# Kernel optimization log

Measured on AMD Instinct MI355X. Metric: run time of the kernel, lower is better.

## Reference

```python
import jax, jax.numpy as jnp
import numpy as np

B, S, H, H2, NH, K, L, V, TOUT, MEL = 16, 256, 384, 1536, 2, 3, 4, 256, 1024, 80


def _ln(x, sb):
    # sb: [2, H] -> (scale, bias)
    m = x.mean(-1, keepdims=True)
    v = x.var(-1, keepdims=True)
    return (x - m) * jax.lax.rsqrt(v + 1e-5) * sb[0] + sb[1]


def _conv1d(x, w, b):
    # x: [B, T, Cin], w: [K, Cin, Cout]
    return jax.lax.conv_general_dilated(x, w, (1,), 'SAME',
                                         dimension_numbers=('NWC', 'WIO', 'NWC')) + b


def _mha(x, w, b):
    # w: [4, H, H] (q, k, v, o), b: [4, H]
    T = x.shape[1]
    dh = H // NH
    q = (x @ w[0] + b[0]).reshape(B, T, NH, dh)
    k = (x @ w[1] + b[1]).reshape(B, T, NH, dh)
    v = (x @ w[2] + b[2]).reshape(B, T, NH, dh)
    s = jnp.einsum('bqhd,bkhd->bhqk', q, k) / np.sqrt(dh).astype(np.float32)
    a = jax.nn.softmax(s, axis=-1)
    o = jnp.einsum('bhqk,bkhd->bqhd', a, v).reshape(B, T, H)
    return o @ w[3] + b[3]


def _fft_block(x, aw, ab, c1w, c1b, c2w, c2b, ln):
    x = _ln(x + _mha(x, aw, ab), ln[0])
    f = _conv1d(jax.nn.relu(_conv1d(x, c1w, c1b)), c2w, c2b)
    return _ln(x + f, ln[1])


def _posenc(x):
    T = x.shape[1]
    pos = jnp.arange(T, dtype=jnp.float32)[:, None]
    den = jnp.exp(-np.log(10000.0) * jnp.arange(0, H, 2, dtype=jnp.float32) / H)
    ang = pos * den[None, :]
    pe = jnp.stack([jnp.sin(ang), jnp.cos(ang)], axis=-1).reshape(T, H)
    return x + pe[None]


def setup_inputs() -> dict:
    key = jax.random.key(0)
    ks = iter(jax.random.split(key, 32))
    sc = 0.02
    inp = {}
    inp['tokens'] = jax.random.randint(next(ks), (B, S), 0, V, dtype=jnp.int32)
    inp['alignes'] = jax.random.randint(next(ks), (B, S), 0, 8).astype(jnp.int64)
    inp['tok_emb'] = jax.random.normal(next(ks), (V, H), jnp.float32) * sc
    for pre in ('enc', 'dec'):
        inp[pre + '_attn_w'] = jax.random.normal(next(ks), (L, 4, H, H), jnp.float32) * sc
        inp[pre + '_attn_b'] = jnp.zeros((L, 4, H), jnp.float32)
        inp[pre + '_conv1_w'] = jax.random.normal(next(ks), (L, K, H, H2), jnp.float32) * sc
        inp[pre + '_conv1_b'] = jnp.zeros((L, H2), jnp.float32)
        inp[pre + '_conv2_w'] = jax.random.normal(next(ks), (L, K, H2, H), jnp.float32) * sc
        inp[pre + '_conv2_b'] = jnp.zeros((L, H), jnp.float32)
        ln = jnp.stack([jnp.ones((L, 2, H)), jnp.zeros((L, 2, H))], axis=2)  # [L,2,2,H]
        inp[pre + '_ln'] = ln.astype(jnp.float32)
    inp['al_conv1_w'] = jax.random.normal(next(ks), (K, H, H), jnp.float32) * sc
    inp['al_conv1_b'] = jnp.zeros((H,), jnp.float32)
    inp['al_conv2_w'] = jax.random.normal(next(ks), (K, H, H), jnp.float32) * sc
    inp['al_conv2_b'] = jnp.zeros((H,), jnp.float32)
    inp['al_ln'] = jnp.stack([jnp.ones((2, H)), jnp.zeros((2, H))], axis=1).astype(jnp.float32)
    inp['al_lin_w'] = jax.random.normal(next(ks), (H, 1), jnp.float32) * sc
    inp['al_lin_b'] = jnp.zeros((1,), jnp.float32)
    inp['dec_lin_w'] = jax.random.normal(next(ks), (H, MEL), jnp.float32) * sc
    inp['dec_lin_b'] = jnp.zeros((MEL,), jnp.float32)
    return inp


def reference(tokens, alignes, tok_emb, enc_attn_w, enc_attn_b, enc_conv1_w,
              enc_conv1_b, enc_conv2_w, enc_conv2_b, enc_ln, dec_attn_w,
              dec_attn_b, dec_conv1_w, dec_conv1_b, dec_conv2_w, dec_conv2_b,
              dec_ln, al_conv1_w, al_conv1_b, al_conv2_w, al_conv2_b, al_ln,
              al_lin_w, al_lin_b, dec_lin_w, dec_lin_b):
    # ---- Encoder ----
    x = tok_emb[tokens] * np.sqrt(H).astype(np.float32)
    x = _posenc(x)
    for i in range(L):
        x = _fft_block(x, enc_attn_w[i], enc_attn_b[i], enc_conv1_w[i],
                       enc_conv1_b[i], enc_conv2_w[i], enc_conv2_b[i], enc_ln[i])
    # ---- Aligner (duration predictor) ----
    h = jax.nn.relu(_conv1d(x, al_conv1_w, al_conv1_b))
    h = _ln(h, al_ln[0])
    h = jax.nn.relu(_conv1d(h, al_conv2_w, al_conv2_b))
    h = _ln(h, al_ln[1])
    length_pred = (h @ al_lin_w + al_lin_b)[..., 0]  # [B, S]
    # ---- Length regulator: repeat_interleave + pad_sequence (static TOUT) ----
    dur = alignes.astype(jnp.int32)
    cum = jnp.cumsum(dur, axis=1)                    # [B, S]
    t = jnp.arange(TOUT, dtype=jnp.int32)
    idx = jax.vmap(lambda c: jnp.searchsorted(c, t, side='right'))(cum)  # [B, TOUT]
    valid = t[None, :] < cum[:, -1:]
    idx = jnp.clip(idx, 0, S - 1)
    expanded = jnp.take_along_axis(x, idx[:, :, None], axis=1)
    expanded = expanded * valid[:, :, None].astype(x.dtype)
    # ---- Decoder ----
    y = _posenc(expanded)
    for i in range(L):
        y = _fft_block(y, dec_attn_w[i], dec_attn_b[i], dec_conv1_w[i],
                       dec_conv1_b[i], dec_conv2_w[i], dec_conv2_b[i], dec_ln[i])
    mel = y @ dec_lin_w + dec_lin_b                  # [B, TOUT, 80]
    return jnp.transpose(mel, (0, 2, 1)), length_pred
```

## Files before the change

### kernel.cpp

```cpp
#include <hip/hip_runtime.h>
#include <cstdint>
#include <cstddef>

#define B_    16
#define S_    256
#define H_    384
#define H2_   1536
#define NH_   2
#define DH_   192
#define TOUT_ 1024
#define MEL_  80
#define L_    4

#define F_BIAS  1
#define F_RES   2
#define F_RELU  4
#define F_STF   8
#define F_STB   16
#define F_TRANS 32

typedef __attribute__((ext_vector_type(8))) short short8;
typedef __attribute__((ext_vector_type(4))) float floatx4;

typedef const __attribute__((address_space(1))) unsigned int* as1p;
typedef __attribute__((address_space(3))) unsigned int* as3p;

__device__ __forceinline__ void gld16(const void* g, void* l) {
  __builtin_amdgcn_global_load_lds((as1p)g, (as3p)l, 16, 0, 0);
}

__device__ __forceinline__ short f2b(float f) {
  union { float f; unsigned u; } v; v.f = f;
  unsigned r = (v.u + 0x7fffu + ((v.u >> 16) & 1u)) >> 16;
  return (short)r;
}

__device__ __forceinline__ float pe_val(int t, int i) {
  int j = i >> 1;
  float den = __expf(-9.210340371976184f * (float)(2 * j) / (float)H_);
  float ang = (float)t * den;
  return (i & 1) ? __cosf(ang) : __sinf(ang);
}

__global__ __launch_bounds__(256) void wtrans_kernel(const float* __restrict__ sa,
                                                     const float* __restrict__ sb,
                                                     int na, int K, int N,
                                                     short* __restrict__ dst) {
  __shared__ float t[32][33];
  int id = blockIdx.z;
  const float* s = (id < na) ? sa + (size_t)id * K * N : sb + (size_t)(id - na) * K * N;
  short* o = dst + (size_t)id * K * N;
  int n0 = blockIdx.x * 32, k0 = blockIdx.y * 32;
  int tx = threadIdx.x & 31, ty = threadIdx.x >> 5;
#pragma unroll
  for (int i = 0; i < 4; ++i)
    t[ty + i * 8][tx] = s[(size_t)(k0 + ty + i * 8) * N + n0 + tx];
  __syncthreads();
#pragma unroll
  for (int i = 0; i < 4; ++i)
    o[(size_t)(n0 + ty + i * 8) * K + k0 + tx] = f2b(t[tx][ty + i * 8]);
}

__global__ void melpad_kernel(const float* __restrict__ w, short* __restrict__ dst) {
  int i = blockIdx.x * 256 + threadIdx.x;
  int n = i / H_, k = i - n * H_;
  dst[i] = (n < MEL_) ? f2b(w[(size_t)k * MEL_ + n]) : (short)0;
}

__global__ void embed_kernel(const int* __restrict__ tokens, const float* __restrict__ emb,
                             float* __restrict__ xf, short* __restrict__ xb) {
  int bs = blockIdx.x;
  int t  = bs & (S_ - 1);
  int tok = tokens[bs];
  const float* e = emb + (size_t)tok * H_;
  float* of = xf + (size_t)bs * H_;
  short* ob = xb + (size_t)bs * H_;
  for (int i = threadIdx.x; i < H_; i += blockDim.x) {
    float v = e[i] * 19.595917942265423f + pe_val(t, i);
    of[i] = v; ob[i] = f2b(v);
  }
}

template<int NTAPS>
__global__ __launch_bounds__(256) void mfma_gemm(
    const short* __restrict__ A, const short* __restrict__ Wt,
    const float* __restrict__ bias, const float* __restrict__ res,
    float* __restrict__ Cf, short* __restrict__ Cb, const short* __restrict__ zbuf,
    int M, int N, int Kd, int T, int Nout, int flags)
{
  constexpr int HB   = NTAPS / 2;
  constexpr int RA   = 128 + NTAPS - 1;
  constexpr int RNDA = (RA + 63) / 64;
  __shared__ __align__(16) short As[RA * 32];
  __shared__ __align__(16) short Bs[NTAPS * 128 * 32];
  const int tid = threadIdx.x;
  const int wave = tid >> 6, lane = tid & 63, quad = lane >> 4, lm = lane & 15;
  const int bm = blockIdx.y * 128, bn = blockIdx.x * 128;
  const int wm = (wave >> 1) * 64, wn = (wave & 1) * 64;
  const int b0 = bm / T, t0 = bm - b0 * T;
  floatx4 acc[4][4] = {};

  for (int k0 = 0; k0 < Kd; k0 += 32) {
#pragma unroll
    for (int j = 0; j < RNDA; ++j) {
      int r0 = (j == RNDA - 1) ? (RA - 64) : j * 64;
      int r = r0 + (tid >> 2);
      int t = t0 - HB + r;
      const short* g = (t >= 0 && t < T)
          ? (A + (size_t)(b0 * T + t) * Kd + k0 + (tid & 3) * 8) : zbuf;
      gld16(g, As + r0 * 32 + wave * 512);
    }
#pragma unroll
    for (int j = 0; j < 2 * NTAPS; ++j) {
      int gi = j * 256 + tid;
      int tap = gi >> 9, rr = (gi >> 2) & 127, ch = gi & 3;
      const short* g = Wt + ((size_t)tap * N + bn + rr) * Kd + k0 + ch * 8;
      gld16(g, Bs + j * 2048 + wave * 512);
    }
    __syncthreads();
#pragma unroll
    for (int tap = 0; tap < NTAPS; ++tap) {
      short8 af[4], bfr[4];
#pragma unroll
      for (int mt = 0; mt < 4; ++mt)
        af[mt] = *(const short8*)(&As[(wm + mt * 16 + lm + tap) * 32 + quad * 8]);
#pragma unroll
      for (int nt = 0; nt < 4; ++nt)
        bfr[nt] = *(const short8*)(&Bs[tap * 4096 + (wn + nt * 16 + lm) * 32 + quad * 8]);
#pragma unroll
      for (int mt = 0; mt < 4; ++mt)
#pragma unroll
        for (int nt = 0; nt < 4; ++nt)
          acc[mt][nt] = __builtin_amdgcn_mfma_f32_16x16x32_bf16(af[mt], bfr[nt],
                                                                acc[mt][nt], 0, 0, 0);
    }
    __syncthreads();
  }

#pragma unroll
  for (int mt = 0; mt < 4; ++mt) {
#pragma unroll
    for (int r2 = 0; r2 < 4; ++r2) {
      int gm = bm + wm + mt * 16 + quad * 4 + r2;
#pragma unroll
      for (int nt = 0; nt < 4; ++nt) {
        int gn = bn + wn + nt * 16 + lm;
        float v = acc[mt][nt][r2];
        if (flags & F_TRANS) {
          if (gn < Nout) {
            if (flags & F_BIAS) v += bias[gn];
            int bb = gm / T, tt = gm - bb * T;
            Cf[((size_t)bb * Nout + gn) * T + tt] = v;
          }
          continue;
        }
        if (flags & F_BIAS) v += bias[gn];
        size_t idx = (size_t)gm * N + gn;
        if (flags & F_RES) v += res[idx];
        if (flags & F_RELU) v = fmaxf(v, 0.f);
        if (flags & F_STF) Cf[idx] = v;
        if (flags & F_STB) Cb[idx] = f2b(v);
      }
    }
  }
}

__global__ __launch_bounds__(256) void vtrans_kernel(const short* __restrict__ qkv,
                                                     short* __restrict__ vt, int T) {
  __shared__ short tile[32][34];
  int b = blockIdx.z, d0 = blockIdx.y * 32, t0 = blockIdx.x * 32;
  int tx = threadIdx.x & 31, ty = threadIdx.x >> 5;
#pragma unroll
  for (int i = 0; i < 4; ++i)
    tile[ty + i * 8][tx] = qkv[(size_t)(b * T + t0 + ty + i * 8) * 1152 + 768 + d0 + tx];
  __syncthreads();
  int h = (d0 >= DH_) ? 1 : 0;
  int dd0 = d0 - h * DH_;
#pragma unroll
  for (int i = 0; i < 4; ++i)
    vt[((size_t)((b * NH_ + h) * DH_) + dd0 + ty + i * 8) * T + t0 + tx] = tile[tx][ty + i * 8];
}

template<int T>
__global__ __launch_bounds__(256) void attn_mfma(const short* __restrict__ qkv,
                                                 const short* __restrict__ vt,
                                                 short* __restrict__ o)
{
  constexpr int PK = T / 64;
  constexpr int PW = T + 8;
  __shared__ __align__(16) short qs[16 * 200];
  __shared__ __align__(16) short P[16 * PW];
  __shared__ float red[4][16];
  const int tid = threadIdx.x;
  const int wave = tid >> 6, lane = tid & 63, quad = lane >> 4, lm = lane & 15;
  const int q0 = blockIdx.x * 16, h = blockIdx.y, b = blockIdx.z;
  const short* qb = qkv + (size_t)b * T * 1152 + h * DH_;
  const short* kb = qb + 384;
  const short* vb = vt + (size_t)(b * NH_ + h) * DH_ * T;

  for (int u = tid; u < 16 * 24; u += 256) {
    int r = u / 24, c = u - r * 24;
    *(int4*)(qs + r * 200 + c * 8) = *(const int4*)(qb + (size_t)(q0 + r) * 1152 + c * 8);
  }
  __syncthreads();

  short8 qf[6];
#pragma unroll
  for (int c6 = 0; c6 < 6; ++c6)
    qf[c6] = *(const short8*)(qs + lm * 200 + c6 * 32 + quad * 8);

  floatx4 sacc[PK];
#pragma unroll
  for (int i = 0; i < PK; ++i) {
    int kt = i * 4 + wave;
    floatx4 a = {0.f, 0.f, 0.f, 0.f};
    const short* kp = kb + (size_t)(kt * 16 + lm) * 1152 + quad * 8;
#pragma unroll
    for (int c6 = 0; c6 < 6; ++c6)
      a = __builtin_amdgcn_mfma_f32_16x16x32_bf16(qf[c6], *(const short8*)(kp + c6 * 32),
                                                  a, 0, 0, 0);
#pragma unroll
    for (int r2 = 0; r2 < 4; ++r2) a[r2] *= 0.07216878364870323f;
    sacc[i] = a;
  }

  float mx[4];
#pragma unroll
  for (int r2 = 0; r2 < 4; ++r2) {
    float m = sacc[0][r2];
#pragma unroll
    for (int i = 1; i < PK; ++i) m = fmaxf(m, sacc[i][r2]);
#pragma unroll
    for (int off = 1; off < 16; off <<= 1) m = fmaxf(m, __shfl_xor(m, off, 64));
    mx[r2] = m;
  }
  if (lm == 0) {
#pragma unroll
    for (int r2 = 0; r2 < 4; ++r2) red[wave][quad * 4 + r2] = mx[r2];
  }
  __syncthreads();
  float gm[4];
#pragma unroll
  for (int r2 = 0; r2 < 4; ++r2) {
    int row = quad * 4 + r2;
    gm[r2] = fmaxf(fmaxf(red[0][row], red[1][row]), fmaxf(red[2][row], red[3][row]));
  }
  __syncthreads();

  float sm[4] = {0.f, 0.f, 0.f, 0.f};
#pragma unroll
  for (int i = 0; i < PK; ++i) {
#pragma unroll
    for (int r2 = 0; r2 < 4; ++r2) {
      float e = __expf(sacc[i][r2] - gm[r2]);
      sm[r2] += e;
      P[(quad * 4 + r2) * PW + (i * 4 + wave) * 16 + lm] = f2b(e);
    }
  }
#pragma unroll
  for (int r2 = 0; r2 < 4; ++r2) {
#pragma unroll
    for (int off = 1; off < 16; off <<= 1) sm[r2] += __shfl_xor(sm[r2], off, 64);
  }
  if (lm == 0) {
#pragma unroll
    for (int r2 = 0; r2 < 4; ++r2) red[wave][quad * 4 + r2] = sm[r2];
  }
  __syncthreads();
  float il[4];
#pragma unroll
  for (int r2 = 0; r2 < 4; ++r2) {
    int row = quad * 4 + r2;
    il[r2] = 1.f / (red[0][row] + red[1][row] + red[2][row] + red[3][row]);
  }

  floatx4 oacc[3] = {};
  for (int kc = 0; kc < T / 32; ++kc) {
    short8 af = *(const short8*)(P + lm * PW + kc * 32 + quad * 8);
#pragma unroll
    for (int dx = 0; dx < 3; ++dx) {
      short8 bf = *(const short8*)(vb + (size_t)((wave + dx * 4) * 16 + lm) * T + kc * 32 + quad * 8);
      oacc[dx] = __builtin_amdgcn_mfma_f32_16x16x32_bf16(af, bf, oacc[dx], 0, 0, 0);
    }
  }
#pragma unroll
  for (int dx = 0; dx < 3; ++dx) {
    int col = h * DH_ + (wave + dx * 4) * 16 + lm;
#pragma unroll
    for (int r2 = 0; r2 < 4; ++r2)
      o[(size_t)(b * T + q0 + quad * 4 + r2) * H_ + col] = f2b(oacc[dx][r2] * il[r2]);
  }
}

__global__ __launch_bounds__(256) void ln_kernel(const float* __restrict__ X,
                                                 const float* __restrict__ sb,
                                                 float* __restrict__ Yf,
                                                 short* __restrict__ Yb, int M)
{
  int row  = blockIdx.x * 4 + (threadIdx.x >> 6);
  int lane = threadIdx.x & 63;
  const float* x = X + (size_t)row * H_;
  float v[6]; float s = 0.f, ss = 0.f;
#pragma unroll
  for (int i = 0; i < 6; ++i) { v[i] = x[lane + i * 64]; s += v[i]; ss += v[i] * v[i]; }
#pragma unroll
  for (int o = 32; o; o >>= 1) { s += __shfl_down(s, o, 64); ss += __shfl_down(ss, o, 64); }
  s = __shfl(s, 0, 64); ss = __shfl(ss, 0, 64);
  float mean = s * (1.0f / H_);
  float var  = ss * (1.0f / H_) - mean * mean;
  float r = rsqrtf(var + 1e-5f);
  float* yf = Yf + (size_t)row * H_;
#pragma unroll
  for (int i = 0; i < 6; ++i) {
    int c = lane + i * 64;
    float y = (v[i] - mean) * r * sb[c] + sb[H_ + c];
    yf[c] = y;
    if (Yb) Yb[(size_t)row * H_ + c] = f2b(y);
  }
}

__global__ void gemv_kernel(const float* __restrict__ A, const float* __restrict__ w,
                            const float* __restrict__ bflt, float* __restrict__ out, int M)
{
  int row  = blockIdx.x * 4 + (threadIdx.x >> 6);
  int lane = threadIdx.x & 63;
  const float* a = A + (size_t)row * H_;
  float s = 0.f;
#pragma unroll
  for (int i = 0; i < 6; ++i) s += a[lane + i * 64] * w[lane + i * 64];
#pragma unroll
  for (int o = 32; o; o >>= 1) s += __shfl_down(s, o, 64);
  if (lane == 0) out[row] = s + bflt[0];
}

__global__ void cumsum_kernel(const int* __restrict__ al, int* __restrict__ cum) {
  int b = threadIdx.x;
  if (b < B_) {
    int acc = 0;
    for (int s = 0; s < S_; ++s) { acc += al[b * S_ + s]; cum[b * S_ + s] = acc; }
  }
}

__global__ void expand_kernel(const float* __restrict__ xe, const int* __restrict__ cum,
                              float* __restrict__ yf, short* __restrict__ yb) {
  int t = blockIdx.x, b = blockIdx.y;
  const int* c = cum + b * S_;
  int lo = 0, hi = S_;
  while (lo < hi) { int mid = (lo + hi) >> 1; if (c[mid] <= t) lo = mid + 1; else hi = mid; }
  int idx = lo < S_ ? lo : S_ - 1;
  bool valid = t < c[S_ - 1];
  const float* src = xe + ((size_t)b * S_ + idx) * H_;
  float* df = yf + ((size_t)b * TOUT_ + t) * H_;
  short* db = yb + ((size_t)b * TOUT_ + t) * H_;
  for (int i = threadIdx.x; i < H_; i += blockDim.x) {
    float v = (valid ? src[i] : 0.f) + pe_val(t, i);
    df[i] = v; db[i] = f2b(v);
  }
}

static inline void gemm(const short* A, const short* Wt, const float* bias, const float* res,
                        float* Cf, short* Cb, const short* zbuf, int M, int N, int Kd, int T,
                        int ntaps, int Nout, int flags, hipStream_t st) {
  dim3 g(N / 128, M / 128);
  if (ntaps == 3)
    mfma_gemm<3><<<g, 256, 0, st>>>(A, Wt, bias, res, Cf, Cb, zbuf, M, N, Kd, T, Nout, flags);
  else
    mfma_gemm<1><<<g, 256, 0, st>>>(A, Wt, bias, res, Cf, Cb, zbuf, M, N, Kd, T, Nout, flags);
}

struct LayerW { const short *attn, *c1, *c2; const float *ab, *c1b, *c2b, *ln; };

static void fft_block(float* x, short* xb, short* qkvb, short* ob, short* vtb, short* h2b,
                      const short* zbuf, const LayerW& w, int T, hipStream_t st)
{
  int M = B_ * T;
  const size_t msz = (size_t)H_ * H_;
  gemm(xb, w.attn, w.ab, nullptr, nullptr, qkvb, zbuf, M, 1152, H_, T, 1, 0, F_BIAS | F_STB, st);
  vtrans_kernel<<<dim3(T / 32, 12, B_), 256, 0, st>>>(qkvb, vtb, T);
  if (T == 256) attn_mfma<256><<<dim3(T / 16, NH_, B_), 256, 0, st>>>(qkvb, vtb, ob);
  else          attn_mfma<1024><<<dim3(T / 16, NH_, B_), 256, 0, st>>>(qkvb, vtb, ob);
  gemm(ob, w.attn + 3 * msz, w.ab + 3 * H_, x, x, nullptr, zbuf, M, H_, H_, T, 1, 0,
       F_BIAS | F_RES | F_STF, st);
  ln_kernel<<<M / 4, 256, 0, st>>>(x, w.ln, x, xb, M);
  gemm(xb, w.c1, w.c1b, nullptr, nullptr, h2b, zbuf, M, H2_, H_, T, 3, 0,
       F_BIAS | F_RELU | F_STB, st);
  gemm(h2b, w.c2, w.c2b, x, x, nullptr, zbuf, M, H_, H2_, T, 3, 0, F_BIAS | F_RES | F_STF, st);
  ln_kernel<<<M / 4, 256, 0, st>>>(x, w.ln + 2 * H_, x, xb, M);
}

extern "C" void kernel_launch(void* const* d_in, const int* in_sizes, int n_in,
                              void* d_out, int out_size, void* d_ws, size_t ws_size,
                              hipStream_t stream)
{
  (void)in_sizes; (void)n_in; (void)out_size; (void)ws_size;
  const int*   tokens      = (const int*)d_in[0];
  const int*   alignes     = (const int*)d_in[1];
  const float* tok_emb     = (const float*)d_in[2];
  const float* enc_attn_w  = (const float*)d_in[3];
  const float* enc_attn_b  = (const float*)d_in[4];
  const float* enc_conv1_w = (const float*)d_in[5];
  const float* enc_conv1_b = (const float*)d_in[6];
  const float* enc_conv2_w = (const float*)d_in[7];
  const float* enc_conv2_b = (const float*)d_in[8];
  const float* enc_ln      = (const float*)d_in[9];
  const float* dec_attn_w  = (const float*)d_in[10];
  const float* dec_attn_b  = (const float*)d_in[11];
  const float* dec_conv1_w = (const float*)d_in[12];
  const float* dec_conv1_b = (const float*)d_in[13];
  const float* dec_conv2_w = (const float*)d_in[14];
  const float* dec_conv2_b = (const float*)d_in[15];
  const float* dec_ln      = (const float*)d_in[16];
  const float* al_c1w      = (const float*)d_in[17];
  const float* al_c1b      = (const float*)d_in[18];
  const float* al_c2w      = (const float*)d_in[19];
  const float* al_c2b      = (const float*)d_in[20];
  const float* al_ln       = (const float*)d_in[21];
  const float* al_lin_w    = (const float*)d_in[22];
  const float* al_lin_b    = (const float*)d_in[23];
  const float* dec_lin_w   = (const float*)d_in[24];
  const float* dec_lin_b   = (const float*)d_in[25];

  char* base = (char*)d_ws;
  size_t off = 0;
  auto alloc = [&](size_t bytes) -> char* {
    char* p = base + off;
    off += (bytes + 255) & ~(size_t)255;
    return p;
  };
  const size_t ME = (size_t)B_ * S_;
  const size_t MD = (size_t)B_ * TOUT_;
  float* xe   = (float*)alloc(ME * H_ * 4);
  short* xeb  = (short*)alloc(ME * H_ * 2);
  float* xd   = (float*)alloc(MD * H_ * 4);
  short* xdb  = (short*)alloc(MD * H_ * 2);
  short* qkvb = (short*)alloc(MD * 1152 * 2);
  short* ob   = (short*)alloc(MD * H_ * 2);
  short* h2b  = (short*)alloc(MD * H2_ * 2);
  short* vtb  = h2b;
  short* wAt  = (short*)alloc((size_t)32 * H_ * H_ * 2);
  short* wAl  = (short*)alloc((size_t)6 * H_ * H_ * 2);
  short* wC1  = (short*)alloc((size_t)24 * H_ * H2_ * 2);
  short* wC2  = (short*)alloc((size_t)24 * H_ * H2_ * 2);
  short* wMel = (short*)alloc((size_t)128 * H_ * 2);
  int*   cum  = (int*)alloc(ME * 4);
  short* zbuf = (short*)alloc(256);
  float* alf  = xd;
  short* alb  = xdb;

  float* mel_out = (float*)d_out;
  float* len_out = mel_out + (size_t)B_ * MEL_ * TOUT_;

  hipMemsetAsync(zbuf, 0, 256, stream);

  wtrans_kernel<<<dim3(12, 12, 32), 256, 0, stream>>>(enc_attn_w, dec_attn_w, 16, H_, H_, wAt);
  wtrans_kernel<<<dim3(12, 12, 6),  256, 0, stream>>>(al_c1w, al_c2w, 3, H_, H_, wAl);
  wtrans_kernel<<<dim3(48, 12, 24), 256, 0, stream>>>(enc_conv1_w, dec_conv1_w, 12, H_, H2_, wC1);
  wtrans_kernel<<<dim3(12, 48, 24), 256, 0, stream>>>(enc_conv2_w, dec_conv2_w, 12, H2_, H_, wC2);
  melpad_kernel<<<dim3(128 * H_ / 256), 256, 0, stream>>>(dec_lin_w, wMel);

  embed_kernel<<<dim3(B_ * S_), 128, 0, stream>>>(tokens, tok_emb, xe, xeb);
  for (int i = 0; i < L_; ++i) {
    LayerW w;
    w.attn = wAt + (size_t)i * 4 * H_ * H_;
    w.c1   = wC1 + (size_t)i * 3 * H_ * H2_;
    w.c2   = wC2 + (size_t)i * 3 * H_ * H2_;
    w.ab   = enc_attn_b + (size_t)i * 4 * H_;
    w.c1b  = enc_conv1_b + (size_t)i * H2_;
    w.c2b  = enc_conv2_b + (size_t)i * H_;
    w.ln   = enc_ln + (size_t)i * 4 * H_;
    fft_block(xe, xeb, qkvb, ob, vtb, h2b, zbuf, w, S_, stream);
  }

  {
    int Ma = B_ * S_;
    gemm(xeb, wAl, al_c1b, nullptr, alf, nullptr, zbuf, Ma, H_, H_, S_, 3, 0,
         F_BIAS | F_RELU | F_STF, stream);
    ln_kernel<<<Ma / 4, 256, 0, stream>>>(alf, al_ln, alf, alb, Ma);
    gemm(alb, wAl + (size_t)3 * H_ * H_, al_c2b, nullptr, alf, nullptr, zbuf, Ma, H_, H_, S_,
         3, 0, F_BIAS | F_RELU | F_STF, stream);
    ln_kernel<<<Ma / 4, 256, 0, stream>>>(alf, al_ln + 2 * H_, alf, (short*)nullptr, Ma);
    gemv_kernel<<<Ma / 4, 256, 0, stream>>>(alf, al_lin_w, al_lin_b, len_out, Ma);
  }

  cumsum_kernel<<<1, 64, 0, stream>>>(alignes, cum);
  expand_kernel<<<dim3(TOUT_, B_), 128, 0, stream>>>(xe, cum, xd, xdb);

  for (int i = 0; i < L_; ++i) {
    LayerW w;
    w.attn = wAt + (size_t)(16 + i * 4) * H_ * H_;
    w.c1   = wC1 + (size_t)(12 + i * 3) * H_ * H2_;
    w.c2   = wC2 + (size_t)(12 + i * 3) * H_ * H2_;
    w.ab   = dec_attn_b + (size_t)i * 4 * H_;
    w.c1b  = dec_conv1_b + (size_t)i * H2_;
    w.c2b  = dec_conv2_b + (size_t)i * H_;
    w.ln   = dec_ln + (size_t)i * 4 * H_;
    fft_block(xd, xdb, qkvb, ob, vtb, h2b, zbuf, w, TOUT_, stream);
  }

  gemm(xdb, wMel, dec_lin_b, nullptr, mel_out, nullptr, zbuf, B_ * TOUT_, 128, H_, TOUT_,
       1, MEL_, F_BIAS | F_TRANS, stream);
}
```

Before: 3.363 ms.

## Replace attention kernel with flash-style online softmax and double-buffered K/V staging

The attention kernel now gives each block 64 queries, with 16 per wave, and streams K and V in 32-key chunks. Each chunk is double-buffered in LDS through async global loads, and the softmax is computed online with a running max and sum per row. The old kernel handled 16 queries per block, read K and V straight from global memory, and held the full score row in LDS. The new layout gives four times more K/V reuse per block, removes the full-row LDS buffer, and overlaps loads with MFMA work. In exchange, each wave holds 12 output accumulators, which raises register pressure, and the block count drops, which may lower occupancy and parallelism for the short encoder sequence.

```diff
diff --git a/kernel.cpp b/kernel.cpp
--- a/kernel.cpp
+++ b/kernel.cpp
@@ -182,113 +182,111 @@
 }
 
 template<int T>
-__global__ __launch_bounds__(256) void attn_mfma(const short* __restrict__ qkv,
-                                                 const short* __restrict__ vt,
-                                                 short* __restrict__ o)
+__global__ __launch_bounds__(256) void attn_flash(const short* __restrict__ qkv,
+                                                  const short* __restrict__ vt,
+                                                  short* __restrict__ o)
 {
-  constexpr int PK = T / 64;
-  constexpr int PW = T + 8;
-  __shared__ __align__(16) short qs[16 * 200];
-  __shared__ __align__(16) short P[16 * PW];
-  __shared__ float red[4][16];
+  constexpr int NKT = T / 32;
+  __shared__ __align__(16) short Kb[2][6144];
+  __shared__ __align__(16) short Vb[2][6144];
+  __shared__ __align__(16) short Pb[4][16 * 40];
   const int tid = threadIdx.x;
   const int wave = tid >> 6, lane = tid & 63, quad = lane >> 4, lm = lane & 15;
-  const int q0 = blockIdx.x * 16, h = blockIdx.y, b = blockIdx.z;
+  const int id = blockIdx.x;
+  const int bh = id & 31, h = bh & 1, b = bh >> 1;
+  const int q0 = (id >> 5) * 64;
   const short* qb = qkv + (size_t)b * T * 1152 + h * DH_;
   const short* kb = qb + 384;
   const short* vb = vt + (size_t)(b * NH_ + h) * DH_ * T;
 
-  for (int u = tid; u < 16 * 24; u += 256) {
-    int r = u / 24, c = u - r * 24;
-    *(int4*)(qs + r * 200 + c * 8) = *(const int4*)(qb + (size_t)(q0 + r) * 1152 + c * 8);
-  }
+  short8 qf[6];
+  {
+    const short* qrow = qb + (size_t)(q0 + wave * 16 + lm) * 1152 + quad * 8;
+#pragma unroll
+    for (int c6 = 0; c6 < 6; ++c6) qf[c6] = *(const short8*)(qrow + c6 * 32);
+  }
+
+  auto stage = [&](int kc, int bi) {
+#pragma unroll
+    for (int j = 0; j < 3; ++j) {
+      int g = j * 256 + tid;
+      int lmg = g & 15, qg = (g >> 4) & 3, ct = g >> 6;
+      int c6 = ct % 6, kt = ct / 6;
+      gld16(kb + (size_t)(kc * 32 + kt * 16 + lmg) * 1152 + c6 * 32 + qg * 8,
+            &Kb[bi][j * 2048 + wave * 512]);
+    }
+#pragma unroll
+    for (int j = 0; j < 3; ++j) {
+      int g = j * 256 + tid;
+      int lmg = g & 15, qg = (g >> 4) & 3, dt = g >> 6;
+      gld16(vb + (size_t)(dt * 16 + lmg) * T + kc * 32 + qg * 8,
+            &Vb[bi][j * 2048 + wave * 512]);
+    }
+  };
+
+  float m_r[4] = {-1e30f, -1e30f, -1e30f, -1e30f};
+  float l_r[4] = {0.f, 0.f, 0.f, 0.f};
+  floatx4 oacc[12] = {};
+
+  stage(0, 0);
   __syncthreads();
 
-  short8 qf[6];
-#pragma unroll
-  for (int c6 = 0; c6 < 6; ++c6)
-    qf[c6] = *(const short8*)(qs + lm * 200 + c6 * 32 + quad * 8);
-
-  floatx4 sacc[PK];
-#pragma unroll
-  for (int i = 0; i < PK; ++i) {
-    int kt = i * 4 + wave;
-    floatx4 a = {0.f, 0.f, 0.f, 0.f};
-    const short* kp = kb + (size_t)(kt * 16 + lm) * 1152 + quad * 8;
-#pragma unroll
-    for (int c6 = 0; c6 < 6; ++c6)
-      a = __builtin_amdgcn_mfma_f32_16x16x32_bf16(qf[c6], *(const short8*)(kp + c6 * 32),
-                                                  a, 0, 0, 0);
-#pragma unroll
-    for (int r2 = 0; r2 < 4; ++r2) a[r2] *= 0.07216878364870323f;
-    sacc[i] = a;
-  }
-
-  float mx[4];
+  for (int kc = 0; kc < NKT; ++kc) {
+    const int cur = kc & 1;
+    if (kc + 1 < NKT) stage(kc + 1, cur ^ 1);
+
+    floatx4 s0 = {0.f, 0.f, 0.f, 0.f}, s1 = {0.f, 0.f, 0.f, 0.f};
+#pragma unroll
+    for (int c6 = 0; c6 < 6; ++c6) {
+      short8 k0f = *(const short8*)(&Kb[cur][(c6 * 64 + quad * 16 + lm) * 8]);
+      short8 k1f = *(const short8*)(&Kb[cur][((6 + c6) * 64 + quad * 16 + lm) * 8]);
+      s0 = __builtin_amdgcn_mfma_f32_16x16x32_bf16(qf[c6], k0f, s0, 0, 0, 0);
+      s1 = __builtin_amdgcn_mfma_f32_16x16x32_bf16(qf[c6], k1f, s1, 0, 0, 0);
+    }
+
+    float al[4];
+#pragma unroll
+    for (int r2 = 0; r2 < 4; ++r2) {
+      float a = s0[r2] * 0.07216878364870323f;
+      float c = s1[r2] * 0.07216878364870323f;
+      float t = fmaxf(a, c);
+#pragma unroll
+      for (int off = 1; off < 16; off <<= 1) t = fmaxf(t, __shfl_xor(t, off, 64));
+      float mn = fmaxf(m_r[r2], t);
+      al[r2] = __expf(m_r[r2] - mn);
+      m_r[r2] = mn;
+      float e0 = __expf(a - mn), e1 = __expf(c - mn);
+      l_r[r2] = al[r2] * l_r[r2] + e0 + e1;
+      Pb[wave][(quad * 4 + r2) * 40 + lm]      = f2b(e0);
+      Pb[wave][(quad * 4 + r2) * 40 + 16 + lm] = f2b(e1);
+    }
+#pragma unroll
+    for (int dt = 0; dt < 12; ++dt) {
+#pragma unroll
+      for (int r2 = 0; r2 < 4; ++r2) oacc[dt][r2] *= al[r2];
+    }
+
+    short8 pf = *(const short8*)(&Pb[wave][lm * 40 + quad * 8]);
+#pragma unroll
+    for (int dt = 0; dt < 12; ++dt) {
+      short8 vf = *(const short8*)(&Vb[cur][(dt * 64 + quad * 16 + lm) * 8]);
+      oacc[dt] = __builtin_amdgcn_mfma_f32_16x16x32_bf16(pf, vf, oacc[dt], 0, 0, 0);
+    }
+    __syncthreads();
+  }
+
 #pragma unroll
   for (int r2 = 0; r2 < 4; ++r2) {
-    float m = sacc[0][r2];
-#pragma unroll
-    for (int i = 1; i < PK; ++i) m = fmaxf(m, sacc[i][r2]);
-#pragma unroll
-    for (int off = 1; off < 16; off <<= 1) m = fmaxf(m, __shfl_xor(m, off, 64));
-    mx[r2] = m;
-  }
-  if (lm == 0) {
-#pragma unroll
-    for (int r2 = 0; r2 < 4; ++r2) red[wave][quad * 4 + r2] = mx[r2];
-  }
-  __syncthreads();
-  float gm[4];
-#pragma unroll
-  for (int r2 = 0; r2 < 4; ++r2) {
-    int row = quad * 4 + r2;
-    gm[r2] = fmaxf(fmaxf(red[0][row], red[1][row]), fmaxf(red[2][row], red[3][row]));
-  }
-  __syncthreads();
-
-  float sm[4] = {0.f, 0.f, 0.f, 0.f};
-#pragma unroll
-  for (int i = 0; i < PK; ++i) {
-#pragma unroll
-    for (int r2 = 0; r2 < 4; ++r2) {
-      float e = __expf(sacc[i][r2] - gm[r2]);
-      sm[r2] += e;
-      P[(quad * 4 + r2) * PW + (i * 4 + wave) * 16 + lm] = f2b(e);
-    }
-  }
-#pragma unroll
-  for (int r2 = 0; r2 < 4; ++r2) {
-#pragma unroll
-    for (int off = 1; off < 16; off <<= 1) sm[r2] += __shfl_xor(sm[r2], off, 64);
-  }
-  if (lm == 0) {
-#pragma unroll
-    for (int r2 = 0; r2 < 4; ++r2) red[wave][quad * 4 + r2] = sm[r2];
-  }
-  __syncthreads();
-  float il[4];
-#pragma unroll
-  for (int r2 = 0; r2 < 4; ++r2) {
-    int row = quad * 4 + r2;
-    il[r2] = 1.f / (red[0][row] + red[1][row] + red[2][row] + red[3][row]);
-  }
-
-  floatx4 oacc[3] = {};
-  for (int kc = 0; kc < T / 32; ++kc) {
-    short8 af = *(const short8*)(P + lm * PW + kc * 32 + quad * 8);
-#pragma unroll
-    for (int dx = 0; dx < 3; ++dx) {
-      short8 bf = *(const short8*)(vb + (size_t)((wave + dx * 4) * 16 + lm) * T + kc * 32 + quad * 8);
-      oacc[dx] = __builtin_amdgcn_mfma_f32_16x16x32_bf16(af, bf, oacc[dx], 0, 0, 0);
-    }
-  }
-#pragma unroll
-  for (int dx = 0; dx < 3; ++dx) {
-    int col = h * DH_ + (wave + dx * 4) * 16 + lm;
+#pragma unroll
+    for (int off = 1; off < 16; off <<= 1) l_r[r2] += __shfl_xor(l_r[r2], off, 64);
+    l_r[r2] = 1.f / l_r[r2];
+  }
+  short* orow = o + (size_t)(b * T + q0 + wave * 16) * H_ + h * DH_;
+#pragma unroll
+  for (int dt = 0; dt < 12; ++dt) {
 #pragma unroll
     for (int r2 = 0; r2 < 4; ++r2)
-      o[(size_t)(b * T + q0 + quad * 4 + r2) * H_ + col] = f2b(oacc[dx][r2] * il[r2]);
+      orow[(size_t)(quad * 4 + r2) * H_ + dt * 16 + lm] = f2b(oacc[dt][r2] * l_r[r2]);
   }
 }
 
@@ -377,8 +375,8 @@
   const size_t msz = (size_t)H_ * H_;
   gemm(xb, w.attn, w.ab, nullptr, nullptr, qkvb, zbuf, M, 1152, H_, T, 1, 0, F_BIAS | F_STB, st);
   vtrans_kernel<<<dim3(T / 32, 12, B_), 256, 0, st>>>(qkvb, vtb, T);
-  if (T == 256) attn_mfma<256><<<dim3(T / 16, NH_, B_), 256, 0, st>>>(qkvb, vtb, ob);
-  else          attn_mfma<1024><<<dim3(T / 16, NH_, B_), 256, 0, st>>>(qkvb, vtb, ob);
+  if (T == 256) attn_flash<256><<<dim3((256 / 64) * 32), 256, 0, st>>>(qkvb, vtb, ob);
+  else          attn_flash<1024><<<dim3((1024 / 64) * 32), 256, 0, st>>>(qkvb, vtb, ob);
   gemm(ob, w.attn + 3 * msz, w.ab + 3 * H_, x, x, nullptr, zbuf, M, H_, H_, T, 1, 0,
        F_BIAS | F_RES | F_STF, st);
   ln_kernel<<<M / 4, 256, 0, st>>>(x, w.ln, x, xb, M);
```

New measurement: 2.978 ms. 11.4% less time.
